# Kernel optimization log

Hardware: AMD Instinct MI355X
Metric: run time of the kernel (lower is better)

Reference implementation:

```python
import jax, jax.numpy as jnp
import numpy as np

EMBED = 512
HEADS = 8
HEAD_DIM = EMBED // HEADS
LN_EPS = 1e-5


def setup_inputs() -> dict:
    key = jax.random.key(0)
    ks = jax.random.split(key, 13)
    B, L = 4, 2048
    s = 1.0 / np.sqrt(EMBED)
    inp = {
        "values": jax.random.normal(ks[0], (B, L, EMBED), dtype=jnp.float32),
        "keys": jax.random.normal(ks[1], (B, L, EMBED), dtype=jnp.float32),
        "query": jax.random.normal(ks[2], (B, L, EMBED), dtype=jnp.float32),
        "Wq": jax.random.uniform(ks[3], (EMBED, EMBED), jnp.float32, -s, s),
        "bq": jax.random.uniform(ks[4], (EMBED,), jnp.float32, -s, s),
        "Wk": jax.random.uniform(ks[5], (EMBED, EMBED), jnp.float32, -s, s),
        "bk": jax.random.uniform(ks[6], (EMBED,), jnp.float32, -s, s),
        "Wv": jax.random.uniform(ks[7], (EMBED, EMBED), jnp.float32, -s, s),
        "bv": jax.random.uniform(ks[8], (EMBED,), jnp.float32, -s, s),
        "Wo": jax.random.uniform(ks[9], (EMBED, EMBED), jnp.float32, -s, s),
        "bo": jax.random.uniform(ks[10], (EMBED,), jnp.float32, -s, s),
        "ln_g": jnp.ones((EMBED,), jnp.float32),
        "ln_b": jnp.zeros((EMBED,), jnp.float32),
    }
    return inp


def reference(values, keys, query, Wq, bq, Wk, bk, Wv, bv, Wo, bo, ln_g, ln_b):
    B, L, _ = query.shape
    # separate QKV linears (torch Linear: x @ W^T + b)
    Q = (query @ Wq.T + bq).reshape(B, L, HEADS, HEAD_DIM)
    K = (keys @ Wk.T + bk).reshape(B, L, HEADS, HEAD_DIM)
    V = (values @ Wv.T + bv).reshape(B, L, HEADS, HEAD_DIM)
    # explicit QK^T scores: [B, H, Q, K]
    scores = jnp.einsum("nqhd,nkhd->nhqk", Q, K) / np.sqrt(HEAD_DIM)
    attn = jax.nn.softmax(scores, axis=-1)
    out = jnp.einsum("nhqk,nkhd->nqhd", attn, V).reshape(B, L, EMBED)
    out = out @ Wo.T + bo
    # residual + LayerNorm (dropout = identity in eval)
    x = out + query
    mu = jnp.mean(x, axis=-1, keepdims=True)
    var = jnp.var(x, axis=-1, keepdims=True)
    return (x - mu) * jax.lax.rsqrt(var + LN_EPS) * ln_g + ln_b
```

## Files before the change

### kernel.cpp

```cpp
#include <hip/hip_runtime.h>

typedef short bf16x8 __attribute__((ext_vector_type(8)));
typedef short s16x4 __attribute__((ext_vector_type(4)));
typedef float f32x4 __attribute__((ext_vector_type(4)));
typedef unsigned int uint4v __attribute__((ext_vector_type(4)));
typedef unsigned int uint2v __attribute__((ext_vector_type(2)));

#define BLM   8192
#define EMB   512
#define LSEQ  2048
#define NHEAD 8
#define HDIM  64

typedef __attribute__((address_space(3))) char lds_ch;
typedef __attribute__((address_space(3))) float lds_f32;

__device__ __forceinline__ unsigned short f2bf(float x) {
    unsigned int u = __builtin_bit_cast(unsigned int, x);
    u += 0x7FFFu + ((u >> 16) & 1u);
    return (unsigned short)(u >> 16);
}

__device__ __forceinline__ unsigned int cvtpk(float lo, float hi) {
    unsigned int r;
    asm("v_cvt_pk_bf16_f32 %0, %1, %2" : "=v"(r) : "v"(lo), "v"(hi));
    return r;
}

__device__ __forceinline__ int swz(int row, int bcol) {
    return row * 128 + (bcol ^ ((row & 7) << 4));
}

#define GLL16(g, l) __builtin_amdgcn_global_load_lds( \
    (const __attribute__((address_space(1))) void*)(g), \
    (__attribute__((address_space(3))) void*)(l), 16, 0, 0)

#define TR16(dst, a, OFF) asm volatile("ds_read_b64_tr_b16 %0, %1 offset:%2" \
    : "=v"(dst) : "v"(a), "n"(OFF))

__global__ __launch_bounds__(256, 3) void k_gemm_qkv(
    const float* __restrict__ Xq, const float* __restrict__ Xk, const float* __restrict__ Xv,
    const float* __restrict__ Wq, const float* __restrict__ Wk, const float* __restrict__ Wv,
    const float* __restrict__ bq, const float* __restrict__ bk, const float* __restrict__ bv,
    unsigned short* __restrict__ Qb, unsigned short* __restrict__ Kb, unsigned short* __restrict__ Vb)
{
    const int z = blockIdx.z;
    const float* X    = (z == 0) ? Xq : (z == 1) ? Xk : Xv;
    const float* W    = (z == 0) ? Wq : (z == 1) ? Wk : Wv;
    const float* bias = (z == 0) ? bq : (z == 1) ? bk : bv;
    unsigned short* out = (z == 0) ? Qb : (z == 1) ? Kb : Vb;
    const float osc = (z == 0) ? 0.125f * 1.44269504088896340736f : 1.0f;

    __shared__ __align__(16) char lds[32768];
    char* As = lds;
    char* Bs = lds + 16384;

    const int tid  = threadIdx.x;
    const int lane = tid & 63;
    const int wave = tid >> 6;
    const int wm = wave >> 1, wn = wave & 1;
    const int lr = lane & 15, lk = lane >> 4;
    const int m0 = blockIdx.x * 128, n0 = blockIdx.y * 128;

    f32x4 acc[4][4] = {};

    const float* pa = X + (size_t)(m0 + (tid >> 4)) * EMB + (tid & 15) * 4;
    const float* pb = W + (size_t)(n0 + (tid >> 4)) * EMB + (tid & 15) * 4;

    float4 ar[8], br[8];
    #pragma unroll
    for (int i = 0; i < 8; ++i) {
        ar[i] = *(const float4*)(pa + (size_t)i * 16 * EMB);
        br[i] = *(const float4*)(pb + (size_t)i * 16 * EMB);
    }
    pa += 64; pb += 64;

    for (int kt = 0; kt < 8; ++kt) {
        __syncthreads();
        #pragma unroll
        for (int i = 0; i < 8; ++i) {
            int f = tid + i * 256;
            int r = f >> 4, c4 = f & 15;
            uint2v p; p.x = cvtpk(ar[i].x, ar[i].y); p.y = cvtpk(ar[i].z, ar[i].w);
            *(uint2v*)(As + swz(r, c4 * 8)) = p;
            uint2v q; q.x = cvtpk(br[i].x, br[i].y); q.y = cvtpk(br[i].z, br[i].w);
            *(uint2v*)(Bs + swz(r, c4 * 8)) = q;
        }
        if (kt < 7) {
            #pragma unroll
            for (int i = 0; i < 8; ++i) {
                ar[i] = *(const float4*)(pa + (size_t)i * 16 * EMB);
                br[i] = *(const float4*)(pb + (size_t)i * 16 * EMB);
            }
            pa += 64; pb += 64;
        }
        __syncthreads();
        #pragma unroll
        for (int ks = 0; ks < 2; ++ks) {
            bf16x8 af[4], bfr[4];
            #pragma unroll
            for (int fm = 0; fm < 4; ++fm)
                af[fm] = *(const bf16x8*)(As + swz(wm * 64 + fm * 16 + lr, ks * 64 + lk * 16));
            #pragma unroll
            for (int fn = 0; fn < 4; ++fn)
                bfr[fn] = *(const bf16x8*)(Bs + swz(wn * 64 + fn * 16 + lr, ks * 64 + lk * 16));
            #pragma unroll
            for (int fm = 0; fm < 4; ++fm)
                #pragma unroll
                for (int fn = 0; fn < 4; ++fn)
                    acc[fm][fn] = __builtin_amdgcn_mfma_f32_16x16x32_bf16(af[fm], bfr[fn], acc[fm][fn], 0, 0, 0);
        }
    }
    #pragma unroll
    for (int fn = 0; fn < 4; ++fn) {
        int n = n0 + wn * 64 + fn * 16 + lr;
        float bv_ = bias[n];
        #pragma unroll
        for (int fm = 0; fm < 4; ++fm) {
            int mb = m0 + wm * 64 + fm * 16 + lk * 4;
            #pragma unroll
            for (int j = 0; j < 4; ++j)
                out[(size_t)(mb + j) * EMB + n] = f2bf((acc[fm][fn][j] + bv_) * osc);
        }
    }
}

__global__ __launch_bounds__(256, 3) void k_gemm_out(
    const unsigned short* __restrict__ AO, const float* __restrict__ Wo,
    const float* __restrict__ bo, const float* __restrict__ res,
    float* __restrict__ Xout)
{
    __shared__ __align__(16) char lds[32768];
    char* As = lds;
    char* Bs = lds + 16384;

    const int tid  = threadIdx.x;
    const int lane = tid & 63;
    const int wave = tid >> 6;
    const int wm = wave >> 1, wn = wave & 1;
    const int lr = lane & 15, lk = lane >> 4;
    const int m0 = blockIdx.x * 128, n0 = blockIdx.y * 128;

    f32x4 acc[4][4] = {};

    const unsigned short* pA = AO + (size_t)(m0 + (tid >> 3)) * EMB + (tid & 7) * 8;
    const float* pB = Wo + (size_t)(n0 + (tid >> 4)) * EMB + (tid & 15) * 4;

    uint4v arA[4]; float4 brB[8];
    #pragma unroll
    for (int i = 0; i < 4; ++i) arA[i] = *(const uint4v*)(pA + (size_t)i * 32 * EMB);
    #pragma unroll
    for (int i = 0; i < 8; ++i) brB[i] = *(const float4*)(pB + (size_t)i * 16 * EMB);
    pA += 64; pB += 64;

    for (int kt = 0; kt < 8; ++kt) {
        __syncthreads();
        #pragma unroll
        for (int i = 0; i < 4; ++i) {
            int f = tid + i * 256;
            int r = f >> 3, c8 = f & 7;
            *(uint4v*)(As + swz(r, c8 * 16)) = arA[i];
        }
        #pragma unroll
        for (int i = 0; i < 8; ++i) {
            int f = tid + i * 256;
            int r = f >> 4, c4 = f & 15;
            uint2v q; q.x = cvtpk(brB[i].x, brB[i].y); q.y = cvtpk(brB[i].z, brB[i].w);
            *(uint2v*)(Bs + swz(r, c4 * 8)) = q;
        }
        if (kt < 7) {
            #pragma unroll
            for (int i = 0; i < 4; ++i) arA[i] = *(const uint4v*)(pA + (size_t)i * 32 * EMB);
            #pragma unroll
            for (int i = 0; i < 8; ++i) brB[i] = *(const float4*)(pB + (size_t)i * 16 * EMB);
            pA += 64; pB += 64;
        }
        __syncthreads();
        #pragma unroll
        for (int ks = 0; ks < 2; ++ks) {
            bf16x8 af[4], bfr[4];
            #pragma unroll
            for (int fm = 0; fm < 4; ++fm)
                af[fm] = *(const bf16x8*)(As + swz(wm * 64 + fm * 16 + lr, ks * 64 + lk * 16));
            #pragma unroll
            for (int fn = 0; fn < 4; ++fn)
                bfr[fn] = *(const bf16x8*)(Bs + swz(wn * 64 + fn * 16 + lr, ks * 64 + lk * 16));
            #pragma unroll
            for (int fm = 0; fm < 4; ++fm)
                #pragma unroll
                for (int fn = 0; fn < 4; ++fn)
                    acc[fm][fn] = __builtin_amdgcn_mfma_f32_16x16x32_bf16(af[fm], bfr[fn], acc[fm][fn], 0, 0, 0);
        }
    }
    #pragma unroll
    for (int fn = 0; fn < 4; ++fn) {
        int n = n0 + wn * 64 + fn * 16 + lr;
        float bv_ = bo[n];
        #pragma unroll
        for (int fm = 0; fm < 4; ++fm) {
            int mb = m0 + wm * 64 + fm * 16 + lk * 4;
            #pragma unroll
            for (int j = 0; j < 4; ++j) {
                size_t idx = (size_t)(mb + j) * EMB + n;
                Xout[idx] = acc[fm][fn][j] + bv_ + res[idx];
            }
        }
    }
}

__global__ __launch_bounds__(256, 4) void k_attn(
    const unsigned short* __restrict__ Qb, const unsigned short* __restrict__ Kb,
    const unsigned short* __restrict__ Vb, unsigned short* __restrict__ AO)
{
    __shared__ __align__(16) char lds[32768];
    lds_ch* LB = (lds_ch*)lds;

    const int tid  = threadIdx.x;
    const int lane = tid & 63;
    const int wave = tid >> 6;
    const int qh   = wave & 1;
    const int kvh  = wave >> 1;
    const int lr = lane & 15, lk = lane >> 4;

    const int bid  = blockIdx.x;
    const int orig = (bid & 7) * 128 + (bid >> 3);
    const int qx = orig & 31, bh = orig >> 5;
    const int b = bh >> 3, h = bh & 7;
    const size_t base = (size_t)b * LSEQ * EMB + h * HDIM;
    const int q0 = qx * 64 + qh * 32;

    const int c0 = tid, c1 = tid + 256;
    auto kcol = [](int c) { int r = c >> 3; return ((c & 7) * 8) ^ ((r & 7) * 8); };
    const unsigned short* srcK0 = Kb + base + (size_t)(c0 >> 3) * EMB + kcol(c0);
    const unsigned short* srcK1 = Kb + base + (size_t)(c1 >> 3) * EMB + kcol(c1);
    auto vsrc = [&](int c) {
        int kv = ((c >> 3) & 15) * 4 + ((c >> 1) & 3);
        int d  = (c >> 7) * 16 + (c & 1) * 8;
        return Vb + base + (size_t)kv * EMB + d;
    };
    const unsigned short* srcV0 = vsrc(c0);
    const unsigned short* srcV1 = vsrc(c1);

    auto stage = [&](int par) {
        lds_ch* kd = LB + par * 8192 + wave * 1024;
        lds_ch* vd = LB + 16384 + par * 8192 + wave * 1024;
        GLL16(srcK0, kd);
        GLL16(srcK1, kd + 4096);
        GLL16(srcV0, vd);
        GLL16(srcV1, vd + 4096);
        srcK0 += 64 * EMB; srcK1 += 64 * EMB;
        srcV0 += 64 * EMB; srcV1 += 64 * EMB;
    };

    bf16x8 qf[2][2];
    #pragma unroll
    for (int qg = 0; qg < 2; ++qg)
        #pragma unroll
        for (int ks = 0; ks < 2; ++ks)
            qf[qg][ks] = *(const bf16x8*)(Qb + base + (size_t)(q0 + qg * 16 + lr) * EMB + ks * 32 + lk * 8);

    f32x4 oaccT[2][4] = {};
    float lrow[2] = {0.f, 0.f};

    lds_ch* vadB = LB + 16384 + kvh * 1024 + lk * 128 + lr * 2;

    stage(0);

    for (int t = 0; t < 32; ++t) {
        const int par = t & 1;
        __syncthreads();
        if (t < 31) stage(par ^ 1);

        char* Kl = lds + par * 8192;
        f32x4 s0[2] = {}, s1[2] = {};
        __builtin_amdgcn_s_setprio(1);
        #pragma unroll
        for (int ks = 0; ks < 2; ++ks) {
            bf16x8 kf0 = *(const bf16x8*)(Kl + swz((kvh * 2 + 0) * 16 + lr, ks * 64 + lk * 16));
            bf16x8 kf1 = *(const bf16x8*)(Kl + swz((kvh * 2 + 1) * 16 + lr, ks * 64 + lk * 16));
            s0[0] = __builtin_amdgcn_mfma_f32_16x16x32_bf16(kf0, qf[0][ks], s0[0], 0, 0, 0);
            s1[0] = __builtin_amdgcn_mfma_f32_16x16x32_bf16(kf0, qf[1][ks], s1[0], 0, 0, 0);
            s0[1] = __builtin_amdgcn_mfma_f32_16x16x32_bf16(kf1, qf[0][ks], s0[1], 0, 0, 0);
            s1[1] = __builtin_amdgcn_mfma_f32_16x16x32_bf16(kf1, qf[1][ks], s1[1], 0, 0, 0);
        }
        __builtin_amdgcn_s_setprio(0);

        #pragma unroll
        for (int blk = 0; blk < 2; ++blk)
            #pragma unroll
            for (int j = 0; j < 4; ++j) {
                s0[blk][j] = __builtin_amdgcn_exp2f(s0[blk][j]);
                s1[blk][j] = __builtin_amdgcn_exp2f(s1[blk][j]);
            }
        {
            f32x4 pc = s0[0] + s0[1];
            lrow[0] += (pc[0] + pc[1]) + (pc[2] + pc[3]);
            f32x4 qc = s1[0] + s1[1];
            lrow[1] += (qc[0] + qc[1]) + (qc[2] + qc[3]);
        }

        uint4v w;
        w.x = cvtpk(s0[0][0], s0[0][1]); w.y = cvtpk(s0[0][2], s0[0][3]);
        w.z = cvtpk(s0[1][0], s0[1][1]); w.w = cvtpk(s0[1][2], s0[1][3]);
        bf16x8 pf0 = __builtin_bit_cast(bf16x8, w);
        uint4v v;
        v.x = cvtpk(s1[0][0], s1[0][1]); v.y = cvtpk(s1[0][2], s1[0][3]);
        v.z = cvtpk(s1[1][0], s1[1][1]); v.w = cvtpk(s1[1][2], s1[1][3]);
        bf16x8 pf1 = __builtin_bit_cast(bf16x8, v);

        lds_ch* vad = vadB + par * 8192;
        uint2v a0, b0, a1, b1, a2, b2, a3, b3;
        __builtin_amdgcn_s_setprio(1);
        TR16(a0, vad, 0);    TR16(b0, vad, 512);
        TR16(a1, vad, 2048); TR16(b1, vad, 2560);
        asm volatile("s_waitcnt lgkmcnt(2)" ::: "memory");
        __builtin_amdgcn_sched_barrier(0);
        {
            uint4v wv; wv.x = a0.x; wv.y = a0.y; wv.z = b0.x; wv.w = b0.y;
            bf16x8 vf = __builtin_bit_cast(bf16x8, wv);
            oaccT[0][0] = __builtin_amdgcn_mfma_f32_16x16x32_bf16(vf, pf0, oaccT[0][0], 0, 0, 0);
            oaccT[1][0] = __builtin_amdgcn_mfma_f32_16x16x32_bf16(vf, pf1, oaccT[1][0], 0, 0, 0);
        }
        TR16(a2, vad, 4096); TR16(b2, vad, 4608);
        asm volatile("s_waitcnt lgkmcnt(2)" ::: "memory");
        __builtin_amdgcn_sched_barrier(0);
        {
            uint4v wv; wv.x = a1.x; wv.y = a1.y; wv.z = b1.x; wv.w = b1.y;
            bf16x8 vf = __builtin_bit_cast(bf16x8, wv);
            oaccT[0][1] = __builtin_amdgcn_mfma_f32_16x16x32_bf16(vf, pf0, oaccT[0][1], 0, 0, 0);
            oaccT[1][1] = __builtin_amdgcn_mfma_f32_16x16x32_bf16(vf, pf1, oaccT[1][1], 0, 0, 0);
        }
        TR16(a3, vad, 6144); TR16(b3, vad, 6656);
        asm volatile("s_waitcnt lgkmcnt(2)" ::: "memory");
        __builtin_amdgcn_sched_barrier(0);
        {
            uint4v wv; wv.x = a2.x; wv.y = a2.y; wv.z = b2.x; wv.w = b2.y;
            bf16x8 vf = __builtin_bit_cast(bf16x8, wv);
            oaccT[0][2] = __builtin_amdgcn_mfma_f32_16x16x32_bf16(vf, pf0, oaccT[0][2], 0, 0, 0);
            oaccT[1][2] = __builtin_amdgcn_mfma_f32_16x16x32_bf16(vf, pf1, oaccT[1][2], 0, 0, 0);
        }
        asm volatile("s_waitcnt lgkmcnt(0)" ::: "memory");
        __builtin_amdgcn_sched_barrier(0);
        {
            uint4v wv; wv.x = a3.x; wv.y = a3.y; wv.z = b3.x; wv.w = b3.y;
            bf16x8 vf = __builtin_bit_cast(bf16x8, wv);
            oaccT[0][3] = __builtin_amdgcn_mfma_f32_16x16x32_bf16(vf, pf0, oaccT[0][3], 0, 0, 0);
            oaccT[1][3] = __builtin_amdgcn_mfma_f32_16x16x32_bf16(vf, pf1, oaccT[1][3], 0, 0, 0);
        }
        __builtin_amdgcn_s_setprio(0);
    }

    __syncthreads();
    lds_f32* red = (lds_f32*)LB;
    if (kvh == 1) {
        lds_f32* dst = red + (qh * 64 + lane) * 34;
        #pragma unroll
        for (int qg = 0; qg < 2; ++qg)
            #pragma unroll
            for (int fd = 0; fd < 4; ++fd)
                #pragma unroll
                for (int j = 0; j < 4; ++j)
                    dst[qg * 16 + fd * 4 + j] = oaccT[qg][fd][j];
        dst[32] = lrow[0]; dst[33] = lrow[1];
    }
    __syncthreads();
    if (kvh == 0) {
        const lds_f32* src = red + (qh * 64 + lane) * 34;
        #pragma unroll
        for (int qg = 0; qg < 2; ++qg)
            #pragma unroll
            for (int fd = 0; fd < 4; ++fd)
                #pragma unroll
                for (int j = 0; j < 4; ++j)
                    oaccT[qg][fd][j] += src[qg * 16 + fd * 4 + j];
        lrow[0] += src[32]; lrow[1] += src[33];

        #pragma unroll
        for (int qg = 0; qg < 2; ++qg) {
            float lr_ = lrow[qg];
            lr_ += __shfl_xor(lr_, 16);
            lr_ += __shfl_xor(lr_, 32);
            float inv = 1.f / lr_;
            unsigned short* aorow = AO + base + (size_t)(q0 + qg * 16 + lr) * EMB;
            #pragma unroll
            for (int fd = 0; fd < 4; ++fd) {
                s16x4 s;
                #pragma unroll
                for (int j = 0; j < 4; ++j) s[j] = (short)f2bf(oaccT[qg][fd][j] * inv);
                *(s16x4*)(aorow + fd * 16 + lk * 4) = s;
            }
        }
    }
}

__global__ __launch_bounds__(64) void k_ln(
    const float* __restrict__ X, const float* __restrict__ g,
    const float* __restrict__ bta, float* __restrict__ out)
{
    const int row = blockIdx.x, lane = threadIdx.x;
    const float* x = X + (size_t)row * EMB;
    float4 a = *(const float4*)(x + lane * 8);
    float4 c = *(const float4*)(x + lane * 8 + 4);
    float s  = a.x + a.y + a.z + a.w + c.x + c.y + c.z + c.w;
    float sq = a.x*a.x + a.y*a.y + a.z*a.z + a.w*a.w + c.x*c.x + c.y*c.y + c.z*c.z + c.w*c.w;
    #pragma unroll
    for (int msk = 1; msk < 64; msk <<= 1) { s += __shfl_xor(s, msk); sq += __shfl_xor(sq, msk); }
    float mu  = s * (1.f / 512.f);
    float var = sq * (1.f / 512.f) - mu * mu;
    float rs  = rsqrtf(var + 1e-5f);
    float4 g0 = *(const float4*)(g + lane * 8), g1 = *(const float4*)(g + lane * 8 + 4);
    float4 b0 = *(const float4*)(bta + lane * 8), b1 = *(const float4*)(bta + lane * 8 + 4);
    float4 o0, o1;
    o0.x = (a.x - mu) * rs * g0.x + b0.x;  o0.y = (a.y - mu) * rs * g0.y + b0.y;
    o0.z = (a.z - mu) * rs * g0.z + b0.z;  o0.w = (a.w - mu) * rs * g0.w + b0.w;
    o1.x = (c.x - mu) * rs * g1.x + b1.x;  o1.y = (c.y - mu) * rs * g1.y + b1.y;
    o1.z = (c.z - mu) * rs * g1.z + b1.z;  o1.w = (c.w - mu) * rs * g1.w + b1.w;
    *(float4*)(out + (size_t)row * EMB + lane * 8) = o0;
    *(float4*)(out + (size_t)row * EMB + lane * 8 + 4) = o1;
}

extern "C" void kernel_launch(void* const* d_in, const int* in_sizes, int n_in,
                              void* d_out, int out_size, void* d_ws, size_t ws_size,
                              hipStream_t stream) {
    const float* values = (const float*)d_in[0];
    const float* keys   = (const float*)d_in[1];
    const float* query  = (const float*)d_in[2];
    const float* Wq = (const float*)d_in[3];  const float* bq = (const float*)d_in[4];
    const float* Wk = (const float*)d_in[5];  const float* bk = (const float*)d_in[6];
    const float* Wv = (const float*)d_in[7];  const float* bv = (const float*)d_in[8];
    const float* Wo = (const float*)d_in[9];  const float* bo = (const float*)d_in[10];
    const float* lng = (const float*)d_in[11];
    const float* lnb = (const float*)d_in[12];

    char* ws = (char*)d_ws;
    unsigned short* Qb = (unsigned short*)(ws);
    unsigned short* Kb = (unsigned short*)(ws + 8u  * 1024 * 1024);
    unsigned short* Vb = (unsigned short*)(ws + 16u * 1024 * 1024);
    unsigned short* AO = (unsigned short*)(ws + 24u * 1024 * 1024);
    float*          Xr = (float*)(ws);

    dim3 gqkv(64, 4, 3);
    k_gemm_qkv<<<gqkv, 256, 0, stream>>>(query, keys, values, Wq, Wk, Wv, bq, bk, bv, Qb, Kb, Vb);
    k_attn<<<1024, 256, 0, stream>>>(Qb, Kb, Vb, AO);
    k_gemm_out<<<dim3(64, 4), 256, 0, stream>>>(AO, Wo, bo, query, Xr);
    k_ln<<<8192, 64, 0, stream>>>(Xr, lng, lnb, (float*)d_out);
}
```

Before: 89.04 us.

## Fuse output projection with residual and LayerNorm; pre-convert Wo to bf16

Replaces the separate output GEMM and LayerNorm kernels with one kernel where each block computes 32 full rows of 512 columns, then does bias, residual and the row mean/variance reduction in registers and LDS. This removes the fp32 intermediate write and reread and one launch. Wo is converted to bf16 once by a small kernel so the GEMM can stream it with direct global-to-LDS loads into double-buffered LDS. The cost is about 137 KB of LDS per block, which limits occupancy to one block per CU. Every block also reloads the whole Wo matrix.

```diff
diff --git a/kernel.cpp b/kernel.cpp
--- a/kernel.cpp
+++ b/kernel.cpp
@@ -125,85 +125,144 @@
     }
 }
 
-__global__ __launch_bounds__(256, 3) void k_gemm_out(
-    const unsigned short* __restrict__ AO, const float* __restrict__ Wo,
+__global__ __launch_bounds__(256) void k_wcvt(
+    const float* __restrict__ W, unsigned short* __restrict__ Wb)
+{
+    int i = (blockIdx.x * 256 + threadIdx.x) * 8;
+    float4 a = *(const float4*)(W + i);
+    float4 b = *(const float4*)(W + i + 4);
+    uint4v p;
+    p.x = cvtpk(a.x, a.y); p.y = cvtpk(a.z, a.w);
+    p.z = cvtpk(b.x, b.y); p.w = cvtpk(b.z, b.w);
+    *(uint4v*)(Wb + i) = p;
+}
+
+__global__ __launch_bounds__(256) void k_gemm_out_ln(
+    const unsigned short* __restrict__ AO, const unsigned short* __restrict__ Wob,
     const float* __restrict__ bo, const float* __restrict__ res,
-    float* __restrict__ Xout)
+    const float* __restrict__ g, const float* __restrict__ bta,
+    float* __restrict__ out)
 {
-    __shared__ __align__(16) char lds[32768];
-    char* As = lds;
-    char* Bs = lds + 16384;
+    __shared__ __align__(16) char lds[140288];
+    lds_ch* LA   = (lds_ch*)lds;
+    lds_ch* LBUF = (lds_ch*)lds + 8192;
+    lds_f32* red = (lds_f32*)((lds_ch*)lds + 139264);
 
     const int tid  = threadIdx.x;
     const int lane = tid & 63;
     const int wave = tid >> 6;
-    const int wm = wave >> 1, wn = wave & 1;
     const int lr = lane & 15, lk = lane >> 4;
-    const int m0 = blockIdx.x * 128, n0 = blockIdx.y * 128;
-
-    f32x4 acc[4][4] = {};
-
-    const unsigned short* pA = AO + (size_t)(m0 + (tid >> 3)) * EMB + (tid & 7) * 8;
-    const float* pB = Wo + (size_t)(n0 + (tid >> 4)) * EMB + (tid & 15) * 4;
-
-    uint4v arA[4]; float4 brB[8];
-    #pragma unroll
-    for (int i = 0; i < 4; ++i) arA[i] = *(const uint4v*)(pA + (size_t)i * 32 * EMB);
-    #pragma unroll
-    for (int i = 0; i < 8; ++i) brB[i] = *(const float4*)(pB + (size_t)i * 16 * EMB);
-    pA += 64; pB += 64;
+
+    const int orig = (blockIdx.x & 7) * 32 + (blockIdx.x >> 3);
+    const int m0 = orig * 32;
+
+    auto kcol = [](int c) { int r = c >> 3; return ((c & 7) * 8) ^ ((r & 7) * 8); };
+    const unsigned short* srcA = AO  + (size_t)(m0 + (tid >> 3)) * EMB + kcol(tid);
+    const unsigned short* srcB = Wob + (size_t)(tid >> 3) * EMB + kcol(tid);
+
+    auto stage = [&](int par) {
+        lds_ch* ad = LA   + par * 4096  + wave * 1024;
+        lds_ch* bd = LBUF + par * 65536 + wave * 1024;
+        GLL16(srcA, ad);
+        #pragma unroll
+        for (int i = 0; i < 16; ++i)
+            GLL16(srcB + (size_t)i * 32 * EMB, bd + i * 4096);
+        srcA += 64; srcB += 64;
+    };
+
+    float bov[8], gv[8], btv[8];
+    #pragma unroll
+    for (int fn = 0; fn < 8; ++fn) {
+        int n = wave * 128 + fn * 16 + lr;
+        bov[fn] = bo[n]; gv[fn] = g[n]; btv[fn] = bta[n];
+    }
+
+    f32x4 acc[2][8] = {};
+
+    stage(0);
 
     for (int kt = 0; kt < 8; ++kt) {
+        const int par = kt & 1;
         __syncthreads();
-        #pragma unroll
-        for (int i = 0; i < 4; ++i) {
-            int f = tid + i * 256;
-            int r = f >> 3, c8 = f & 7;
-            *(uint4v*)(As + swz(r, c8 * 16)) = arA[i];
-        }
-        #pragma unroll
-        for (int i = 0; i < 8; ++i) {
-            int f = tid + i * 256;
-            int r = f >> 4, c4 = f & 15;
-            uint2v q; q.x = cvtpk(brB[i].x, brB[i].y); q.y = cvtpk(brB[i].z, brB[i].w);
-            *(uint2v*)(Bs + swz(r, c4 * 8)) = q;
-        }
-        if (kt < 7) {
-            #pragma unroll
-            for (int i = 0; i < 4; ++i) arA[i] = *(const uint4v*)(pA + (size_t)i * 32 * EMB);
-            #pragma unroll
-            for (int i = 0; i < 8; ++i) brB[i] = *(const float4*)(pB + (size_t)i * 16 * EMB);
-            pA += 64; pB += 64;
-        }
-        __syncthreads();
+        if (kt < 7) stage(par ^ 1);
+
+        char* Asb = (char*)lds + par * 4096;
+        char* Bsb = (char*)lds + 8192 + par * 65536;
         #pragma unroll
         for (int ks = 0; ks < 2; ++ks) {
-            bf16x8 af[4], bfr[4];
-            #pragma unroll
-            for (int fm = 0; fm < 4; ++fm)
-                af[fm] = *(const bf16x8*)(As + swz(wm * 64 + fm * 16 + lr, ks * 64 + lk * 16));
-            #pragma unroll
-            for (int fn = 0; fn < 4; ++fn)
-                bfr[fn] = *(const bf16x8*)(Bs + swz(wn * 64 + fn * 16 + lr, ks * 64 + lk * 16));
-            #pragma unroll
-            for (int fm = 0; fm < 4; ++fm)
+            bf16x8 af[2], bf[8];
+            #pragma unroll
+            for (int fm = 0; fm < 2; ++fm)
+                af[fm] = *(const bf16x8*)(Asb + swz(fm * 16 + lr, ks * 64 + lk * 16));
+            #pragma unroll
+            for (int fn = 0; fn < 8; ++fn)
+                bf[fn] = *(const bf16x8*)(Bsb + swz(wave * 128 + fn * 16 + lr, ks * 64 + lk * 16));
+            #pragma unroll
+            for (int fm = 0; fm < 2; ++fm)
                 #pragma unroll
-                for (int fn = 0; fn < 4; ++fn)
-                    acc[fm][fn] = __builtin_amdgcn_mfma_f32_16x16x32_bf16(af[fm], bfr[fn], acc[fm][fn], 0, 0, 0);
-        }
-    }
-    #pragma unroll
-    for (int fn = 0; fn < 4; ++fn) {
-        int n = n0 + wn * 64 + fn * 16 + lr;
-        float bv_ = bo[n];
-        #pragma unroll
-        for (int fm = 0; fm < 4; ++fm) {
-            int mb = m0 + wm * 64 + fm * 16 + lk * 4;
+                for (int fn = 0; fn < 8; ++fn)
+                    acc[fm][fn] = __builtin_amdgcn_mfma_f32_16x16x32_bf16(af[fm], bf[fn], acc[fm][fn], 0, 0, 0);
+        }
+    }
+
+    float ssum[2][4], sqsum[2][4];
+    #pragma unroll
+    for (int fm = 0; fm < 2; ++fm) {
+        #pragma unroll
+        for (int j = 0; j < 4; ++j) {
+            int rr = fm * 16 + lk * 4 + j;
+            const float* rrow = res + (size_t)(m0 + rr) * EMB + wave * 128 + lr;
+            float s = 0.f, sq = 0.f;
+            #pragma unroll
+            for (int fn = 0; fn < 8; ++fn) {
+                float x = acc[fm][fn][j] + bov[fn] + rrow[fn * 16];
+                acc[fm][fn][j] = x;
+                s += x; sq += x * x;
+            }
+            ssum[fm][j] = s; sqsum[fm][j] = sq;
+        }
+    }
+    #pragma unroll
+    for (int fm = 0; fm < 2; ++fm)
+        #pragma unroll
+        for (int j = 0; j < 4; ++j) {
+            float s = ssum[fm][j], sq = sqsum[fm][j];
+            #pragma unroll
+            for (int msk = 1; msk < 16; msk <<= 1) {
+                s  += __shfl_xor(s,  msk);
+                sq += __shfl_xor(sq, msk);
+            }
+            ssum[fm][j] = s; sqsum[fm][j] = sq;
+        }
+    if (lr == 0) {
+        #pragma unroll
+        for (int fm = 0; fm < 2; ++fm)
             #pragma unroll
             for (int j = 0; j < 4; ++j) {
-                size_t idx = (size_t)(mb + j) * EMB + n;
-                Xout[idx] = acc[fm][fn][j] + bv_ + res[idx];
-            }
+                int rr = fm * 16 + lk * 4 + j;
+                red[(wave * 32 + rr) * 2 + 0] = ssum[fm][j];
+                red[(wave * 32 + rr) * 2 + 1] = sqsum[fm][j];
+            }
+    }
+    __syncthreads();
+    #pragma unroll
+    for (int fm = 0; fm < 2; ++fm) {
+        #pragma unroll
+        for (int j = 0; j < 4; ++j) {
+            int rr = fm * 16 + lk * 4 + j;
+            float tot = 0.f, totsq = 0.f;
+            #pragma unroll
+            for (int w2 = 0; w2 < 4; ++w2) {
+                tot   += red[(w2 * 32 + rr) * 2 + 0];
+                totsq += red[(w2 * 32 + rr) * 2 + 1];
+            }
+            float mu  = tot * (1.f / 512.f);
+            float var = totsq * (1.f / 512.f) - mu * mu;
+            float rs  = rsqrtf(var + 1e-5f);
+            float* orow = out + (size_t)(m0 + rr) * EMB + wave * 128 + lr;
+            #pragma unroll
+            for (int fn = 0; fn < 8; ++fn)
+                orow[fn * 16] = (acc[fm][fn][j] - mu) * rs * gv[fn] + btv[fn];
         }
     }
 }
@@ -393,32 +452,6 @@
     }
 }
 
-__global__ __launch_bounds__(64) void k_ln(
-    const float* __restrict__ X, const float* __restrict__ g,
-    const float* __restrict__ bta, float* __restrict__ out)
-{
-    const int row = blockIdx.x, lane = threadIdx.x;
-    const float* x = X + (size_t)row * EMB;
-    float4 a = *(const float4*)(x + lane * 8);
-    float4 c = *(const float4*)(x + lane * 8 + 4);
-    float s  = a.x + a.y + a.z + a.w + c.x + c.y + c.z + c.w;
-    float sq = a.x*a.x + a.y*a.y + a.z*a.z + a.w*a.w + c.x*c.x + c.y*c.y + c.z*c.z + c.w*c.w;
-    #pragma unroll
-    for (int msk = 1; msk < 64; msk <<= 1) { s += __shfl_xor(s, msk); sq += __shfl_xor(sq, msk); }
-    float mu  = s * (1.f / 512.f);
-    float var = sq * (1.f / 512.f) - mu * mu;
-    float rs  = rsqrtf(var + 1e-5f);
-    float4 g0 = *(const float4*)(g + lane * 8), g1 = *(const float4*)(g + lane * 8 + 4);
-    float4 b0 = *(const float4*)(bta + lane * 8), b1 = *(const float4*)(bta + lane * 8 + 4);
-    float4 o0, o1;
-    o0.x = (a.x - mu) * rs * g0.x + b0.x;  o0.y = (a.y - mu) * rs * g0.y + b0.y;
-    o0.z = (a.z - mu) * rs * g0.z + b0.z;  o0.w = (a.w - mu) * rs * g0.w + b0.w;
-    o1.x = (c.x - mu) * rs * g1.x + b1.x;  o1.y = (c.y - mu) * rs * g1.y + b1.y;
-    o1.z = (c.z - mu) * rs * g1.z + b1.z;  o1.w = (c.w - mu) * rs * g1.w + b1.w;
-    *(float4*)(out + (size_t)row * EMB + lane * 8) = o0;
-    *(float4*)(out + (size_t)row * EMB + lane * 8 + 4) = o1;
-}
-
 extern "C" void kernel_launch(void* const* d_in, const int* in_sizes, int n_in,
                               void* d_out, int out_size, void* d_ws, size_t ws_size,
                               hipStream_t stream) {
@@ -437,11 +470,11 @@
     unsigned short* Kb = (unsigned short*)(ws + 8u  * 1024 * 1024);
     unsigned short* Vb = (unsigned short*)(ws + 16u * 1024 * 1024);
     unsigned short* AO = (unsigned short*)(ws + 24u * 1024 * 1024);
-    float*          Xr = (float*)(ws);
+    unsigned short* Wob = (unsigned short*)(ws);
 
     dim3 gqkv(64, 4, 3);
     k_gemm_qkv<<<gqkv, 256, 0, stream>>>(query, keys, values, Wq, Wk, Wv, bq, bk, bv, Qb, Kb, Vb);
     k_attn<<<1024, 256, 0, stream>>>(Qb, Kb, Vb, AO);
-    k_gemm_out<<<dim3(64, 4), 256, 0, stream>>>(AO, Wo, bo, query, Xr);
-    k_ln<<<8192, 64, 0, stream>>>(Xr, lng, lnb, (float*)d_out);
-}
+    k_wcvt<<<128, 256, 0, stream>>>(Wo, Wob);
+    k_gemm_out_ln<<<256, 256, 0, stream>>>(AO, Wob, bo, query, lng, lnb, (float*)d_out);
+}
```

New measurement: 86.41 us (median of 2 runs). -3.0%, faster.
